# Kernel optimization log

Hardware: AMD Instinct MI355X
Metric: run time of the kernel (lower is better)

The kernel has to match this reference:

```python
import jax, jax.numpy as jnp
import numpy as np

B, CIN, COUT, KH, KW, H, W = 32, 64, 64, 3, 3, 128, 128
STRIDE = (1, 1)
PADDING = [(1, 1), (1, 1)]


def setup_inputs() -> dict:
    key = jax.random.key(0)
    k1, k2, k3, k4 = jax.random.split(key, 4)
    x = jax.random.normal(k1, (B, CIN, H, W), dtype=jnp.float32)
    cov = jax.random.uniform(k2, (B,), dtype=jnp.float32)
    # kaiming-normal fan_out init: std = sqrt(2 / (cout*kh*kw))
    std = np.sqrt(2.0 / (COUT * KH * KW)).astype(np.float32)
    W_0 = jax.random.normal(k3, (COUT, CIN, KH, KW), dtype=jnp.float32) * std
    W_1 = jax.random.normal(k4, (COUT, CIN, KH, KW), dtype=jnp.float32) * std
    return {"x": x, "cov": cov, "W_0": W_0, "W_1": W_1}


def reference(x, cov, W_0, W_1):
    # per-sample kernel: W_0 + cov[i] * W_1  -> [B, COUT, CIN, KH, KW]
    kernels = W_0[None] + cov[:, None, None, None, None] * W_1[None]

    def conv_one(xi, k):
        # xi: [CIN, H, W], k: [COUT, CIN, KH, KW]
        out = jax.lax.conv_general_dilated(
            xi[None], k, window_strides=STRIDE, padding=PADDING,
            dimension_numbers=("NCHW", "OIHW", "NCHW"))
        return out[0]

    return jax.vmap(conv_one)(x, kernels)  # [B, COUT, H, W]
```

## Files before the change

kernel.cpp:

```cpp
#include <hip/hip_runtime.h>
#include <stdint.h>

#define B_   32
#define CIN  64
#define COUT 64
#define H_   128
#define W_   128
#define WP   130
#define CIH  32

typedef __bf16 bf16x8 __attribute__((ext_vector_type(8)));
typedef float  f32x4  __attribute__((ext_vector_type(4)));

__device__ inline unsigned int f2bf(float f) {
  union { float f; unsigned u; } uf; uf.f = f;
  unsigned u = uf.u;
  unsigned r = 0x7FFFu + ((u >> 16) & 1u);
  return (u + r) >> 16;
}

__device__ inline unsigned int pk2(float a, float b) {
  unsigned short x = __builtin_bit_cast(unsigned short, (__bf16)a);
  unsigned short y = __builtin_bit_cast(unsigned short, (__bf16)b);
  return (unsigned int)x | ((unsigned int)y << 16);
}

__global__ __launch_bounds__(256) void prep_w(const float* __restrict__ W0,
                                              const float* __restrict__ W1,
                                              const float* __restrict__ cov,
                                              unsigned short* __restrict__ Wb) {
  int g  = blockIdx.x * 256 + threadIdx.x;
  int ci = g & 63;
  int co = (g >> 6) & 63;
  int v  = g >> 12;
  int b  = v / 9;
  int p  = v - b * 9;
  int widx = (co * CIN + ci) * 9 + p;
  float val = W0[widx] + cov[b] * W1[widx];
  Wb[g] = (unsigned short)f2bf(val);
}

__device__ inline void stage_phase(const float* __restrict__ X,
                                   unsigned short* dst_row,
                                   int b, int ih, int ci0, int l, int w0,
                                   bool first) {
  if (first) {
    unsigned int* d32 = (unsigned int*)dst_row;
    if (l < 16) d32[l] = 0u;
    else if (l < 32) d32[129 * 16 + (l - 16)] = 0u;
  }
  if (ih < 0 || ih > 127) {
    if (first) {
      int4 z = {0, 0, 0, 0};
      int4* d = (int4*)(dst_row + CIH);
      #pragma unroll
      for (int k = 0; k < 8; k++) d[k * 64 + l] = z;
    }
    return;
  }
  const float* src = X + (((size_t)b * CIN + ci0) * H_ + ih) * W_ + w0;
  const int hw = H_ * W_;
  int wp0 = w0 + 1, wp1 = w0 + 2;
  int sw0 = (wp0 >> 1) & 3, sw1 = (wp1 >> 1) & 3;
  unsigned short* base0 = dst_row + wp0 * CIH;
  unsigned short* base1 = dst_row + wp1 * CIH;
  #pragma unroll 2
  for (int g = 0; g < CIH; g += 4) {
    const float* s = src + (size_t)g * hw;
    float2 a0 = *(const float2*)(s);
    float2 a1 = *(const float2*)(s + hw);
    float2 a2 = *(const float2*)(s + 2 * hw);
    float2 a3 = *(const float2*)(s + 3 * hw);
    uint2 v0, v1;
    v0.x = pk2(a0.x, a1.x); v0.y = pk2(a2.x, a3.x);
    v1.x = pk2(a0.y, a1.y); v1.y = pk2(a2.y, a3.y);
    int o = g >> 3, pos = g & 7;
    *(uint2*)(base0 + ((o ^ sw0) << 3) + pos) = v0;
    *(uint2*)(base1 + ((o ^ sw1) << 3) + pos) = v1;
  }
}

__global__ __launch_bounds__(256, 4) void conv_fused(
    const float* __restrict__ X,
    const unsigned short* __restrict__ Wb,
    float* __restrict__ out) {
  __shared__ __align__(16) unsigned short Xs[4 * WP * CIH];

  int tile = blockIdx.x;
  int b  = tile >> 6;
  int h0 = (tile & 63) * 2;
  int t  = threadIdx.x;
  int wv = t >> 6;
  int l  = t & 63;

  unsigned short* dst_row = Xs + wv * (WP * CIH);
  int ih = h0 - 1 + wv;
  int w0 = l << 1;

  int lh = l & 15;
  int q  = l >> 4;
  int rbase[4], cbase[4];
  #pragma unroll
  for (int nt = 0; nt < 4; nt++) {
    int p = wv * 64 + nt * 16 + lh;
    rbase[nt] = p >> 7;
    cbase[nt] = p & 127;
  }

  const unsigned short* wbase = Wb + (size_t)b * 9 * 64 * 64;

  f32x4 acc[4][4];

  stage_phase(X, dst_row, b, ih, 0, l, w0, true);
  __syncthreads();

  #pragma unroll
  for (int i = 0; i < 4; i++)
    #pragma unroll
    for (int j = 0; j < 4; j++) acc[i][j] = (f32x4){0.f, 0.f, 0.f, 0.f};

  #pragma unroll 1
  for (int ph = 0; ph < 2; ph++) {
    for (int kh = 0; kh < 3; kh++) {
      #pragma unroll
      for (int kw = 0; kw < 3; kw++) {
        const unsigned short* wk = wbase + (kh * 3 + kw) * 4096 + ph * 32;
        bf16x8 af[4], bfr[4];
        #pragma unroll
        for (int mt = 0; mt < 4; mt++)
          af[mt] = *(const bf16x8*)(wk + (mt * 16 + lh) * 64 + q * 8);
        #pragma unroll
        for (int nt = 0; nt < 4; nt++) {
          int r = rbase[nt] + kh;
          int c = cbase[nt] + kw;
          int slot = q ^ ((c >> 1) & 3);
          bfr[nt] = *(const bf16x8*)(Xs + (r * WP + c) * CIH + slot * 8);
        }
        __builtin_amdgcn_s_setprio(1);
        #pragma unroll
        for (int mt = 0; mt < 4; mt++)
          #pragma unroll
          for (int nt = 0; nt < 4; nt++)
            acc[mt][nt] = __builtin_amdgcn_mfma_f32_16x16x32_bf16(
                af[mt], bfr[nt], acc[mt][nt], 0, 0, 0);
        __builtin_amdgcn_s_setprio(0);
      }
    }
    if (ph == 0) {
      __syncthreads();
      stage_phase(X, dst_row, b, ih, 32, l, w0, false);
      __syncthreads();
    }
  }

  #pragma unroll
  for (int mt = 0; mt < 4; mt++) {
    int coutb = mt * 16 + q * 4;
    #pragma unroll
    for (int nt = 0; nt < 4; nt++) {
      int oh = h0 + rbase[nt];
      int ow = cbase[nt];
      #pragma unroll
      for (int r = 0; r < 4; r++) {
        int cout = coutb + r;
        out[(((size_t)b * COUT + cout) * H_ + oh) * W_ + ow] = acc[mt][nt][r];
      }
    }
  }
}

extern "C" void kernel_launch(void* const* d_in, const int* in_sizes, int n_in,
                              void* d_out, int out_size, void* d_ws, size_t ws_size,
                              hipStream_t stream) {
  const float* x   = (const float*)d_in[0];
  const float* cov = (const float*)d_in[1];
  const float* W0  = (const float*)d_in[2];
  const float* W1  = (const float*)d_in[3];
  float* out = (float*)d_out;

  unsigned short* Wb = (unsigned short*)d_ws;

  prep_w   <<<dim3(4608), dim3(256), 0, stream>>>(W0, W1, cov, Wb);
  conv_fused<<<dim3(2048), dim3(256), 0, stream>>>(x, Wb, out);
}
```

Measured before the change: 308.6 us.

## Stage all input channels once and split output channels across 8 waves

Each block now uses 512 threads (8 waves) and stages all 64 input channels of the 4 halo rows into LDS in a single pass. This removes the mid-kernel resync and the second staging phase. The 8 waves split the 64 output channels into two halves, so each wave holds a 2x4 accumulator tile instead of 4x4. That lowers register pressure and adds parallelism for latency hiding. In exchange, LDS per block doubles (about 66KB), which may limit how many blocks fit per CU, and the kw/ck loops are no longer unrolled.

Measured after the change: 300.2 us. 1.03x faster.

```diff
diff --git a/kernel.cpp b/kernel.cpp
--- a/kernel.cpp
+++ b/kernel.cpp
@@ -7,7 +7,6 @@
 #define H_   128
 #define W_   128
 #define WP   130
-#define CIH  32
 
 typedef __bf16 bf16x8 __attribute__((ext_vector_type(8)));
 typedef float  f32x4  __attribute__((ext_vector_type(4)));
@@ -40,51 +39,11 @@
   Wb[g] = (unsigned short)f2bf(val);
 }
 
-__device__ inline void stage_phase(const float* __restrict__ X,
-                                   unsigned short* dst_row,
-                                   int b, int ih, int ci0, int l, int w0,
-                                   bool first) {
-  if (first) {
-    unsigned int* d32 = (unsigned int*)dst_row;
-    if (l < 16) d32[l] = 0u;
-    else if (l < 32) d32[129 * 16 + (l - 16)] = 0u;
-  }
-  if (ih < 0 || ih > 127) {
-    if (first) {
-      int4 z = {0, 0, 0, 0};
-      int4* d = (int4*)(dst_row + CIH);
-      #pragma unroll
-      for (int k = 0; k < 8; k++) d[k * 64 + l] = z;
-    }
-    return;
-  }
-  const float* src = X + (((size_t)b * CIN + ci0) * H_ + ih) * W_ + w0;
-  const int hw = H_ * W_;
-  int wp0 = w0 + 1, wp1 = w0 + 2;
-  int sw0 = (wp0 >> 1) & 3, sw1 = (wp1 >> 1) & 3;
-  unsigned short* base0 = dst_row + wp0 * CIH;
-  unsigned short* base1 = dst_row + wp1 * CIH;
-  #pragma unroll 2
-  for (int g = 0; g < CIH; g += 4) {
-    const float* s = src + (size_t)g * hw;
-    float2 a0 = *(const float2*)(s);
-    float2 a1 = *(const float2*)(s + hw);
-    float2 a2 = *(const float2*)(s + 2 * hw);
-    float2 a3 = *(const float2*)(s + 3 * hw);
-    uint2 v0, v1;
-    v0.x = pk2(a0.x, a1.x); v0.y = pk2(a2.x, a3.x);
-    v1.x = pk2(a0.y, a1.y); v1.y = pk2(a2.y, a3.y);
-    int o = g >> 3, pos = g & 7;
-    *(uint2*)(base0 + ((o ^ sw0) << 3) + pos) = v0;
-    *(uint2*)(base1 + ((o ^ sw1) << 3) + pos) = v1;
-  }
-}
-
-__global__ __launch_bounds__(256, 4) void conv_fused(
+__global__ __launch_bounds__(512, 4) void conv_fused(
     const float* __restrict__ X,
     const unsigned short* __restrict__ Wb,
     float* __restrict__ out) {
-  __shared__ __align__(16) unsigned short Xs[4 * WP * CIH];
+  __shared__ __align__(16) unsigned short Xs[4 * WP * 64];
 
   int tile = blockIdx.x;
   int b  = tile >> 6;
@@ -93,52 +52,87 @@
   int wv = t >> 6;
   int l  = t & 63;
 
-  unsigned short* dst_row = Xs + wv * (WP * CIH);
-  int ih = h0 - 1 + wv;
-  int w0 = l << 1;
+  {
+    int r    = wv >> 1;
+    int half = wv & 1;
+    unsigned short* dst_row = Xs + r * (WP * 64);
+    unsigned int* d32 = (unsigned int*)(dst_row + half * (129 * 64));
+    if (l < 32) d32[l] = 0u;
 
+    int ih = h0 - 1 + r;
+    if (ih < 0 || ih > 127) {
+      int4 z = {0, 0, 0, 0};
+      int4* d = (int4*)(dst_row + 64);
+      #pragma unroll
+      for (int k = 0; k < 8; k++) d[half * 512 + k * 64 + l] = z;
+    } else {
+      const int hw = H_ * W_;
+      const float* src = X + (((size_t)b * CIN + half * 32) * H_ + ih) * W_ + (l << 1);
+      int wp0 = (l << 1) + 1, wp1 = (l << 1) + 2;
+      unsigned short* base0 = Xs + r * (WP * 64) + wp0 * 64;
+      unsigned short* base1 = Xs + r * (WP * 64) + wp1 * 64;
+      int s0 = wp0 & 7, s1 = wp1 & 7;
+      #pragma unroll 2
+      for (int g = 0; g < 32; g += 4) {
+        const float* s = src + (size_t)g * hw;
+        float2 a0 = *(const float2*)(s);
+        float2 a1 = *(const float2*)(s + hw);
+        float2 a2 = *(const float2*)(s + 2 * hw);
+        float2 a3 = *(const float2*)(s + 3 * hw);
+        uint2 v0, v1;
+        v0.x = pk2(a0.x, a1.x); v0.y = pk2(a2.x, a3.x);
+        v1.x = pk2(a0.y, a1.y); v1.y = pk2(a2.y, a3.y);
+        int ci = half * 32 + g;
+        int o = ci >> 3, pos = ci & 7;
+        *(uint2*)(base0 + (((o ^ s0) << 3) + pos)) = v0;
+        *(uint2*)(base1 + (((o ^ s1) << 3) + pos)) = v1;
+      }
+    }
+  }
+  __syncthreads();
+
+  int wvp = wv & 3;
+  int wv2 = wv >> 2;
   int lh = l & 15;
   int q  = l >> 4;
+
   int rbase[4], cbase[4];
   #pragma unroll
   for (int nt = 0; nt < 4; nt++) {
-    int p = wv * 64 + nt * 16 + lh;
+    int p = wvp * 64 + nt * 16 + lh;
     rbase[nt] = p >> 7;
     cbase[nt] = p & 127;
   }
 
-  const unsigned short* wbase = Wb + (size_t)b * 9 * 64 * 64;
-
-  f32x4 acc[4][4];
-
-  stage_phase(X, dst_row, b, ih, 0, l, w0, true);
-  __syncthreads();
-
+  f32x4 acc[2][4];
   #pragma unroll
-  for (int i = 0; i < 4; i++)
+  for (int i = 0; i < 2; i++)
     #pragma unroll
     for (int j = 0; j < 4; j++) acc[i][j] = (f32x4){0.f, 0.f, 0.f, 0.f};
 
+  const unsigned short* wbase = Wb + (size_t)b * 9 * 4096 + (size_t)(wv2 * 32) * 64;
+
   #pragma unroll 1
-  for (int ph = 0; ph < 2; ph++) {
-    for (int kh = 0; kh < 3; kh++) {
-      #pragma unroll
-      for (int kw = 0; kw < 3; kw++) {
-        const unsigned short* wk = wbase + (kh * 3 + kw) * 4096 + ph * 32;
-        bf16x8 af[4], bfr[4];
+  for (int kh = 0; kh < 3; kh++) {
+    #pragma unroll 1
+    for (int kw = 0; kw < 3; kw++) {
+      const unsigned short* wk = wbase + (kh * 3 + kw) * 4096;
+      #pragma unroll 1
+      for (int ck = 0; ck < 2; ck++) {
+        bf16x8 af[2], bfr[4];
         #pragma unroll
-        for (int mt = 0; mt < 4; mt++)
-          af[mt] = *(const bf16x8*)(wk + (mt * 16 + lh) * 64 + q * 8);
+        for (int mt = 0; mt < 2; mt++)
+          af[mt] = *(const bf16x8*)(wk + (mt * 16 + lh) * 64 + ck * 32 + q * 8);
         #pragma unroll
         for (int nt = 0; nt < 4; nt++) {
           int r = rbase[nt] + kh;
           int c = cbase[nt] + kw;
-          int slot = q ^ ((c >> 1) & 3);
-          bfr[nt] = *(const bf16x8*)(Xs + (r * WP + c) * CIH + slot * 8);
+          int blk = (ck * 4 + q) ^ (c & 7);
+          bfr[nt] = *(const bf16x8*)(Xs + (r * WP + c) * 64 + blk * 8);
         }
         __builtin_amdgcn_s_setprio(1);
         #pragma unroll
-        for (int mt = 0; mt < 4; mt++)
+        for (int mt = 0; mt < 2; mt++)
           #pragma unroll
           for (int nt = 0; nt < 4; nt++)
             acc[mt][nt] = __builtin_amdgcn_mfma_f32_16x16x32_bf16(
@@ -146,16 +140,11 @@
         __builtin_amdgcn_s_setprio(0);
       }
     }
-    if (ph == 0) {
-      __syncthreads();
-      stage_phase(X, dst_row, b, ih, 32, l, w0, false);
-      __syncthreads();
-    }
   }
 
   #pragma unroll
-  for (int mt = 0; mt < 4; mt++) {
-    int coutb = mt * 16 + q * 4;
+  for (int mt = 0; mt < 2; mt++) {
+    int coutb = wv2 * 32 + mt * 16 + q * 4;
     #pragma unroll
     for (int nt = 0; nt < 4; nt++) {
       int oh = h0 + rbase[nt];
@@ -181,5 +170,5 @@
   unsigned short* Wb = (unsigned short*)d_ws;
 
   prep_w   <<<dim3(4608), dim3(256), 0, stream>>>(W0, W1, cov, Wb);
-  conv_fused<<<dim3(2048), dim3(256), 0, stream>>>(x, Wb, out);
+  conv_fused<<<dim3(2048), dim3(512), 0, stream>>>(x, Wb, out);
 }
```
